# Performance work log

Hardware: AMD Instinct MI355X
Metric: run time of the kernel (lower is better)

Reference implementation:

```python
import jax, jax.numpy as jnp
import numpy as np

D_MODEL = 1024
NHEAD = 16
HEAD_DIM = D_MODEL // NHEAD
DFF = 4096
EPS = 1e-5


def _layernorm(x, g, b):
    mu = jnp.mean(x, axis=-1, keepdims=True)
    var = jnp.mean(jnp.square(x - mu), axis=-1, keepdims=True)
    return (x - mu) * jax.lax.rsqrt(var + EPS) * g + b


def setup_inputs() -> dict:
    key = jax.random.key(0)
    ks = jax.random.split(key, 20)
    B, S = 2, 2048
    s = 0.02
    inp = {
        "src": jax.random.normal(ks[0], (B, S, D_MODEL), jnp.float32),
        "recompute_idx": jnp.sort(jax.random.randint(ks[1], (409,), 0, S)),
        "cached_k": jax.random.normal(ks[2], (B, NHEAD, S, HEAD_DIM), jnp.float32),
        "cached_v": jax.random.normal(ks[3], (B, NHEAD, S, HEAD_DIM), jnp.float32),
        "Wq": jax.random.normal(ks[4], (D_MODEL, D_MODEL), jnp.float32) * s,
        "bq": jnp.zeros((D_MODEL,), jnp.float32),
        "Wk": jax.random.normal(ks[5], (D_MODEL, D_MODEL), jnp.float32) * s,
        "bk": jnp.zeros((D_MODEL,), jnp.float32),
        "Wv": jax.random.normal(ks[6], (D_MODEL, D_MODEL), jnp.float32) * s,
        "bv": jnp.zeros((D_MODEL,), jnp.float32),
        "Wo": jax.random.normal(ks[7], (D_MODEL, D_MODEL), jnp.float32) * s,
        "bo": jnp.zeros((D_MODEL,), jnp.float32),
        "W1": jax.random.normal(ks[8], (DFF, D_MODEL), jnp.float32) * s,
        "b1": jnp.zeros((DFF,), jnp.float32),
        "W2": jax.random.normal(ks[9], (D_MODEL, DFF), jnp.float32) * s,
        "b2": jnp.zeros((D_MODEL,), jnp.float32),
        "g1": jnp.ones((D_MODEL,), jnp.float32),
        "beta1": jnp.zeros((D_MODEL,), jnp.float32),
        "g2": jnp.ones((D_MODEL,), jnp.float32),
        "beta2": jnp.zeros((D_MODEL,), jnp.float32),
    }
    return inp


def reference(src, recompute_idx, cached_k, cached_v, Wq, bq, Wk, bk, Wv, bv,
              Wo, bo, W1, b1, W2, b2, g1, beta1, g2, beta2):
    B, S, D = src.shape
    H, hd = NHEAD, HEAD_DIM

    # Q for all tokens
    q = (src @ Wq.T + bq).reshape(B, S, H, hd).transpose(0, 2, 1, 3)  # [B,H,S,hd]

    # K/V recomputed only for selected tokens, scattered over cached KV
    src_rec = src[:, recompute_idx, :]  # [B,R,D]
    R = src_rec.shape[1]
    k_rec = (src_rec @ Wk.T + bk).reshape(B, R, H, hd).transpose(0, 2, 1, 3)
    v_rec = (src_rec @ Wv.T + bv).reshape(B, R, H, hd).transpose(0, 2, 1, 3)
    k_full = cached_k.at[:, :, recompute_idx, :].set(k_rec)  # [B,H,S,hd]
    v_full = cached_v.at[:, :, recompute_idx, :].set(v_rec)

    # attention over mixed cached/fresh KV
    scores = jnp.einsum('bhqd,bhkd->bhqk', q, k_full) / np.sqrt(hd).astype(src.dtype)
    probs = jax.nn.softmax(scores, axis=-1)
    attn = jnp.einsum('bhqk,bhkd->bhqd', probs, v_full)
    attn = attn.transpose(0, 2, 1, 3).reshape(B, S, D)
    attn = attn @ Wo.T + bo

    x = _layernorm(src + attn, g1, beta1)
    ff = jax.nn.relu(x @ W1.T + b1) @ W2.T + b2
    x = _layernorm(x + ff, g2, beta2)
    return x
```

## Files before the change

kernel.cpp:

```cpp
#include <hip/hip_runtime.h>
#include <hip/hip_bf16.h>

typedef __attribute__((ext_vector_type(4))) float f32x4;
typedef __attribute__((ext_vector_type(16))) float f32x16;
typedef __attribute__((ext_vector_type(8))) short s16x8;
typedef __attribute__((ext_vector_type(4))) short s16x4;
typedef __attribute__((ext_vector_type(2))) short s16x2;

typedef __attribute__((address_space(1))) const unsigned int guint;
typedef __attribute__((address_space(3))) unsigned int luint;

#define D_MODEL 1024
#define NHEAD 16
#define HEAD_DIM 64
#define DFF 4096
#define SEQ 2048
#define BATCH 2
#define QSCALE 0.18033688011112042f

__device__ __forceinline__ float b2f(short s) {
  union { unsigned int u; float f; } v;
  v.u = ((unsigned int)(unsigned short)s) << 16;
  return v.f;
}
__device__ __forceinline__ short f2b(float f) {
  __hip_bfloat16 h = __float2bfloat16(f);
  return *reinterpret_cast<short*>(&h);
}
__device__ __forceinline__ s16x8 cvt8(f32x4 a, f32x4 b) {
  s16x8 r;
  #pragma unroll
  for (int i = 0; i < 4; ++i) { r[i] = f2b(a[i]); r[i + 4] = f2b(b[i]); }
  return r;
}

template<int MODE>
__global__ __launch_bounds__(512, 2)
void gemm_ff8(const short* __restrict__ A, const short* __restrict__ W,
              const float* __restrict__ bias, short* __restrict__ out,
              int N, int K,
              short* __restrict__ pB, short* __restrict__ pC,
              short* __restrict__ pD)
{
  __shared__ short Al[2][16384];
  __shared__ short Bl[2][16384];

  const int tid  = threadIdx.x;
  const int lane = tid & 63, wave = tid >> 6;
  const int l31 = lane & 31, hi = lane >> 5;
  const int wm = (wave >> 2) * 128;
  const int wn = (wave & 3) * 64;

  const int nwg = gridDim.x * gridDim.y;
  int lid = blockIdx.y * gridDim.x + blockIdx.x;
  if ((nwg & 7) == 0) lid = (lid & 7) * (nwg >> 3) + (lid >> 3);
  const int bn = lid % gridDim.x, bm = lid / gridDim.x;

  const int Keff = (MODE == 1) ? (K >> 2) : K;
  const int kOff = (MODE == 1) ? (int)blockIdx.z * Keff : 0;

  const int srow = tid >> 3;
  const int scol = (((tid & 7) ^ ((tid >> 3) & 7)) * 8);
  const short* gA = A + ((long)(bm * 256) + srow) * K + kOff + scol;
  const short* gW = W + ((long)(bn * 256) + srow) * K + kOff + scol;
  const long slotG = 64L * K;

  auto stage = [&](int buf, int slot, int k0) {
    luint* dA = (luint*)((short*)Al + buf * 16384 + slot * 4096 + wave * 512);
    luint* dB = (luint*)((short*)Bl + buf * 16384 + slot * 4096 + wave * 512);
    __builtin_amdgcn_global_load_lds((guint*)(gA + slot * slotG + k0), dA, 16, 0, 0);
    __builtin_amdgcn_global_load_lds((guint*)(gW + slot * slotG + k0), dB, 16, 0, 0);
  };

  const int sw = l31 & 7;

  f32x16 acc[4][2] = {};

  #pragma unroll
  for (int s = 0; s < 4; ++s) stage(0, s, 0);

  const int nt = Keff / 64;
  int cur = 0;
  for (int t = 0; t < nt; ++t) {
    const int k1 = (t + 1) * 64;
    if (t + 1 < nt) {
      stage(cur ^ 1, 0, k1);
      asm volatile("s_waitcnt vmcnt(2)" ::: "memory");
    } else {
      asm volatile("s_waitcnt vmcnt(0)" ::: "memory");
    }
    __builtin_amdgcn_s_barrier();
    __builtin_amdgcn_sched_barrier(0);

    const short* Abuf = (const short*)Al + cur * 16384;
    const short* Bbuf = (const short*)Bl + cur * 16384;

    #pragma unroll
    for (int half = 0; half < 2; ++half) {
      s16x8 av[4][2], bv2[2][2];
      #pragma unroll
      for (int mf = 0; mf < 4; ++mf) {
        const int row = wm + mf * 32 + l31;
        #pragma unroll
        for (int k2 = 0; k2 < 2; ++k2) {
          const int kk = half * 2 + k2;
          av[mf][k2] = *(const s16x8*)(Abuf + row * 64 + (((kk * 2 + hi) ^ sw) << 3));
        }
      }
      #pragma unroll
      for (int nf = 0; nf < 2; ++nf) {
        const int row = wn + nf * 32 + l31;
        #pragma unroll
        for (int k2 = 0; k2 < 2; ++k2) {
          const int kk = half * 2 + k2;
          bv2[nf][k2] = *(const s16x8*)(Bbuf + row * 64 + (((kk * 2 + hi) ^ sw) << 3));
        }
      }
      if (t + 1 < nt) {
        stage(cur ^ 1, half * 2 + 1, k1);
        if (half == 1) stage(cur ^ 1, 2, k1);
      }

      __builtin_amdgcn_s_setprio(1);
      #pragma unroll
      for (int k2 = 0; k2 < 2; ++k2)
        #pragma unroll
        for (int mf = 0; mf < 4; ++mf)
          #pragma unroll
          for (int nf = 0; nf < 2; ++nf)
            acc[mf][nf] = __builtin_amdgcn_mfma_f32_32x32x16_bf16(
                av[mf][k2], bv2[nf][k2], acc[mf][nf], 0, 0, 0);
      __builtin_amdgcn_s_setprio(0);
    }

    __builtin_amdgcn_sched_barrier(0);
    __builtin_amdgcn_s_barrier();
    cur ^= 1;
  }

  short* oz = out;
  if (MODE == 1) {
    const int z = blockIdx.z;
    oz = (z == 0) ? out : (z == 1) ? pB : (z == 2) ? pC : pD;
  }
  #pragma unroll
  for (int mf = 0; mf < 4; ++mf) {
    #pragma unroll
    for (int nf = 0; nf < 2; ++nf) {
      const int gn = bn * 256 + wn + nf * 32 + l31;
      const float bvv = (MODE == 0) ? bias[gn] : 0.f;
      #pragma unroll
      for (int reg = 0; reg < 16; ++reg) {
        const int gm = bm * 256 + wm + mf * 32 + (reg & 3) + 8 * (reg >> 2) + 4 * hi;
        float v = acc[mf][nf][reg] + bvv;
        if (MODE == 0) v = v > 0.f ? v : 0.f;
        oz[(long)gm * N + gn] = f2b(v);
      }
    }
  }
}

template<int MODE, int BN, bool AF32, bool WF32>
__global__ __launch_bounds__(256, 3)
void gemm_nt(const void* __restrict__ Av, const void* __restrict__ Wv,
             const float* __restrict__ bias, short* __restrict__ out,
             int M, int N, int K,
             const int* __restrict__ idx, int R,
             const float* __restrict__ bias2, const float* __restrict__ bias3,
             short* __restrict__ pB, short* __restrict__ pC,
             short* __restrict__ pD)
{
  constexpr bool GLDS = (!AF32 && !WF32);
  constexpr int NI = BN / 32;

  const float* Af = (const float*)Av;
  const short* Ab = (const short*)Av;
  const float* Wf = (const float*)Wv;
  const short* Wb = (const short*)Wv;

  const int tid  = threadIdx.x;
  const int lane = tid & 63, wave = tid >> 6;
  const int g = lane >> 4, l15 = lane & 15;
  const int wm = (wave & 1) * 64, wn = (wave >> 1) * (BN / 2);

  const int nwg = gridDim.x * gridDim.y;
  int lid = blockIdx.y * gridDim.x + blockIdx.x;
  if ((nwg & 7) == 0) lid = (lid & 7) * (nwg >> 3) + (lid >> 3);
  const int bn = lid % gridDim.x;
  const int bm0 = lid / gridDim.x;

  int task = 0, bm = bm0, Mt = M;
  if (MODE == 8) {
    if (bm0 < 32)      { task = 0; bm = bm0;      Mt = M; }
    else if (bm0 < 39) { task = 1; bm = bm0 - 32; Mt = BATCH * R; }
    else               { task = 2; bm = bm0 - 39; Mt = BATCH * R; }
  }

  f32x4 acc[4][NI] = {};

  if constexpr (GLDS) {
    __shared__ short As[2][128][32];
    __shared__ short Bs[2][BN][32];

    const short* Wbase = Wb + ((MODE == 8) ? ((size_t)task << 20) : 0);
    const int nz   = (MODE == 6) ? gridDim.z : 1;
    const int Keff = K / nz;
    const int kOff = (MODE == 6) ? (int)blockIdx.z * Keff : 0;

    const int rA0 = wave * 16 + (lane >> 2);
    const int rA1 = rA0 + 64;
    const int cs = (((lane & 3) ^ ((lane >> 3) & 3)) * 8);

    auto arow = [&](int r) -> long {
      const int gm = bm * 128 + r;
      const int am = gm < Mt ? gm : Mt - 1;
      if (MODE == 8 && task > 0) {
        const int b0 = am / R;
        return (long)(b0 * SEQ + idx[am - b0 * R]);
      }
      return am;
    };
    const long aR0 = arow(rA0), aR1 = arow(rA1);
    const long wR0 = (long)bn * BN + rA0;

    const short* gA0 = Ab + aR0 * K + kOff + cs;
    const short* gA1 = Ab + aR1 * K + kOff + cs;
    const short* gB0 = Wbase + wR0 * K + kOff + cs;
    const short* gB1 = nullptr;
    if constexpr (BN == 128) gB1 = Wbase + ((long)bn * BN + rA1) * K + kOff + cs;

    auto stage = [&](int buf, int k0) {
      luint* lA0 = (luint*)((short*)As + buf * 4096 + wave * 512);
      luint* lA1 = (luint*)((short*)As + buf * 4096 + (4 + wave) * 512);
      luint* lB0 = (luint*)((short*)Bs + buf * (BN * 32) + wave * 512);
      __builtin_amdgcn_global_load_lds((guint*)(gA0 + k0), lA0, 16, 0, 0);
      __builtin_amdgcn_global_load_lds((guint*)(gA1 + k0), lA1, 16, 0, 0);
      __builtin_amdgcn_global_load_lds((guint*)(gB0 + k0), lB0, 16, 0, 0);
      if constexpr (BN == 128) {
        luint* lB1 = (luint*)((short*)Bs + buf * (BN * 32) + (4 + wave) * 512);
        __builtin_amdgcn_global_load_lds((guint*)(gB1 + k0), lB1, 16, 0, 0);
      }
    };

    const int rcol = ((g ^ ((l15 >> 1) & 3)) * 8);

    const int nt = Keff / 32;
    stage(0, 0);
    int cur = 0;
    for (int t = 0; t < nt; ++t) {
      if (t + 1 < nt) {
        stage(cur ^ 1, (t + 1) * 32);
        if constexpr (BN == 128) asm volatile("s_waitcnt vmcnt(4)" ::: "memory");
        else                     asm volatile("s_waitcnt vmcnt(3)" ::: "memory");
      } else {
        asm volatile("s_waitcnt vmcnt(0)" ::: "memory");
      }
      __builtin_amdgcn_s_barrier();
      __builtin_amdgcn_sched_barrier(0);

      s16x8 af[4], bf4[NI];
      #pragma unroll
      for (int mi = 0; mi < 4; ++mi)
        af[mi] = *(const s16x8*)&As[cur][wm + mi * 16 + l15][rcol];
      #pragma unroll
      for (int ni = 0; ni < NI; ++ni)
        bf4[ni] = *(const s16x8*)&Bs[cur][wn + ni * 16 + l15][rcol];
      #pragma unroll
      for (int mi = 0; mi < 4; ++mi)
        #pragma unroll
        for (int ni = 0; ni < NI; ++ni)
          acc[mi][ni] = __builtin_amdgcn_mfma_f32_16x16x32_bf16(af[mi], bf4[ni], acc[mi][ni], 0, 0, 0);

      __builtin_amdgcn_sched_barrier(0);
      __builtin_amdgcn_s_barrier();
      cur ^= 1;
    }
  } else {
    __shared__ short As[128][40];
    __shared__ short Bs[128][40];
    const int r0 = tid >> 1, c0 = (tid & 1) * 16;
    const int gm0 = bm * 128 + r0;
    const int am0 = gm0 < M ? gm0 : M - 1;
    long aRow0;
    if (MODE == 3 || MODE == 4) {
      const int b0 = am0 / R;
      aRow0 = (long)(b0 * SEQ + idx[am0 - b0 * R]);
    } else {
      aRow0 = am0;
    }
    const long wRow0 = bn * 128 + r0;

    for (int k0 = 0; k0 < K; k0 += 32) {
      __syncthreads();
      if (AF32) {
        f32x4 a0 = *(const f32x4*)(Af + aRow0 * K + k0 + c0);
        f32x4 a1 = *(const f32x4*)(Af + aRow0 * K + k0 + c0 + 4);
        f32x4 a2 = *(const f32x4*)(Af + aRow0 * K + k0 + c0 + 8);
        f32x4 a3 = *(const f32x4*)(Af + aRow0 * K + k0 + c0 + 12);
        *(s16x8*)&As[r0][c0]     = cvt8(a0, a1);
        *(s16x8*)&As[r0][c0 + 8] = cvt8(a2, a3);
      } else {
        *(s16x8*)&As[r0][c0]     = *(const s16x8*)(Ab + aRow0 * K + k0 + c0);
        *(s16x8*)&As[r0][c0 + 8] = *(const s16x8*)(Ab + aRow0 * K + k0 + c0 + 8);
      }
      if (WF32) {
        f32x4 w0 = *(const f32x4*)(Wf + wRow0 * K + k0 + c0);
        f32x4 w1 = *(const f32x4*)(Wf + wRow0 * K + k0 + c0 + 4);
        f32x4 w2 = *(const f32x4*)(Wf + wRow0 * K + k0 + c0 + 8);
        f32x4 w3 = *(const f32x4*)(Wf + wRow0 * K + k0 + c0 + 12);
        *(s16x8*)&Bs[r0][c0]     = cvt8(w0, w1);
        *(s16x8*)&Bs[r0][c0 + 8] = cvt8(w2, w3);
      } else {
        *(s16x8*)&Bs[r0][c0]     = *(const s16x8*)(Wb + wRow0 * K + k0 + c0);
        *(s16x8*)&Bs[r0][c0 + 8] = *(const s16x8*)(Wb + wRow0 * K + k0 + c0 + 8);
      }
      __syncthreads();

      s16x8 af[4], bf4[4];
      #pragma unroll
      for (int mi = 0; mi < 4; ++mi)
        af[mi] = *(const s16x8*)&As[wm + mi * 16 + l15][g * 8];
      #pragma unroll
      for (int ni = 0; ni < 4; ++ni)
        bf4[ni] = *(const s16x8*)&Bs[wn + ni * 16 + l15][g * 8];
      #pragma unroll
      for (int mi = 0; mi < 4; ++mi)
        #pragma unroll
        for (int ni = 0; ni < 4; ++ni)
          acc[mi][ni % NI] = __builtin_amdgcn_mfma_f32_16x16x32_bf16(af[mi], bf4[ni], acc[mi][ni % NI], 0, 0, 0);
    }
  }

  short* outz = out;
  if (MODE == 6) {
    const int z = blockIdx.z;
    outz = (z == 0) ? out : (z == 1) ? pB : (z == 2) ? pC : pD;
  }

  #pragma unroll
  for (int mi = 0; mi < 4; ++mi) {
    #pragma unroll
    for (int ni = 0; ni < NI; ++ni) {
      const int gn = bn * BN + wn + ni * 16 + l15;
      float bv;
      if (MODE == 6)      bv = 0.f;
      else if (MODE == 8) bv = (task == 0) ? bias[gn] : (task == 1) ? bias2[gn] : bias3[gn];
      else                bv = bias[gn];
      #pragma unroll
      for (int r = 0; r < 4; ++r) {
        const int gm = bm * 128 + wm + mi * 16 + g * 4 + r;
        if (MODE == 8) { if (gm >= Mt) continue; }
        else           { if (gm >= M)  continue; }
        float v = acc[mi][ni][r] + bv;
        if (MODE == 1) v = v > 0.f ? v : 0.f;
        if (MODE == 2) v *= QSCALE;
        if (MODE == 0 || MODE == 1) {
          out[(long)gm * N + gn] = f2b(v);
        } else if (MODE == 2) {
          const int b = gm >> 11, s = gm & (SEQ - 1);
          const int h = gn >> 6, d = gn & 63;
          out[(((long)(b * NHEAD + h)) * SEQ + s) * 64 + d] = f2b(v);
        } else if (MODE == 3) {
          const int b = gm / R, s = idx[gm - b * R];
          const int h = gn >> 6, d = gn & 63;
          out[(((long)(b * NHEAD + h)) * SEQ + s) * 64 + d] = f2b(v);
        } else if (MODE == 4) {
          const int b = gm / R, s = idx[gm - b * R];
          const int h = gn >> 6, d = gn & 63;
          out[(((long)(b * NHEAD + h)) * 64 + d) * SEQ + s] = f2b(v);
        } else if (MODE == 6) {
          outz[(long)gm * N + gn] = f2b(v);
        } else {
          const int h = gn >> 6, d = gn & 63;
          if (task == 0) {
            const int b = gm >> 11, s = gm & (SEQ - 1);
            out[(((long)(b * NHEAD + h)) * SEQ + s) * 64 + d] = f2b(v * QSCALE);
          } else if (task == 1) {
            const int b = gm / R, s = idx[gm - b * R];
            (out + (1L << 22))[(((long)(b * NHEAD + h)) * SEQ + s) * 64 + d] = f2b(v);
          } else {
            const int b = gm / R, s = idx[gm - b * R];
            (out + (1L << 23))[(((long)(b * NHEAD + h)) * 64 + d) * SEQ + s] = f2b(v);
          }
        }
      }
    }
  }
}

__global__ __launch_bounds__(256, 2)
void attn_fwd(const short* __restrict__ Q, const short* __restrict__ Kf,
              const short* __restrict__ Vt, short* __restrict__ out)
{
  __shared__ short Kl[2][64][64];
  __shared__ short Vl[2][64][64];

  const int tid  = threadIdx.x;
  const int lane = tid & 63, w = tid >> 6;
  const int g = lane >> 4, l15 = lane & 15;
  const int bh = blockIdx.x;
  const int qt = blockIdx.y;
  const int b  = bh >> 4, h = bh & 15;

  const long base = (long)bh * SEQ * 64;
  const int  q0   = qt * 128 + w * 32;

  s16x8 qf[2][2];
  #pragma unroll
  for (int mi = 0; mi < 2; ++mi)
    #pragma unroll
    for (int c = 0; c < 2; ++c)
      qf[mi][c] = *(const s16x8*)(Q + base + (long)(q0 + mi * 16 + l15) * 64 + c * 32 + g * 8);

  f32x4 o[2][4] = {};
  f32x4 os[2] = {};

  s16x8 ones;
  #pragma unroll
  for (int j = 0; j < 8; ++j) ones[j] = (short)0x3F80;

  auto ldsw = [](short (*buf)[64], int row, int slot) -> short* {
    return (short*)((char*)&buf[0][0] + row * 128 + ((slot ^ (row & 7)) << 4));
  };

  const int bo0 = w * 2048 + lane * 16;
  const int bo1 = bo0 + 1024;
  const int row0 = bo0 >> 7, ss0 = (((bo0 >> 4) & 7) ^ (row0 & 7));
  const int row1 = bo1 >> 7, ss1 = (((bo1 >> 4) & 7) ^ (row1 & 7));
  const short* gK0 = Kf + base + row0 * 64 + ss0 * 8;
  const short* gK1 = Kf + base + row1 * 64 + ss1 * 8;
  const short* gV0 = Vt + base + (long)row0 * SEQ + ss0 * 8;
  const short* gV1 = Vt + base + (long)row1 * SEQ + ss1 * 8;

  auto stage = [&](int buf, int t) {
    char* kb8 = (char*)&Kl[buf][0][0] + w * 2048;
    char* vb8 = (char*)&Vl[buf][0][0] + w * 2048;
    __builtin_amdgcn_global_load_lds((guint*)(gK0 + t * 4096), (luint*)kb8, 16, 0, 0);
    __builtin_amdgcn_global_load_lds((guint*)(gK1 + t * 4096), (luint*)(kb8 + 1024), 16, 0, 0);
    __builtin_amdgcn_global_load_lds((guint*)(gV0 + t * 64), (luint*)vb8, 16, 0, 0);
    __builtin_amdgcn_global_load_lds((guint*)(gV1 + t * 64), (luint*)(vb8 + 1024), 16, 0, 0);
  };

  stage(0, 0);
  int cur = 0;
  for (int t = 0; t < SEQ / 64; ++t) {
    if (t + 1 < SEQ / 64) {
      stage(cur ^ 1, t + 1);
      asm volatile("s_waitcnt vmcnt(4)" ::: "memory");
    } else {
      asm volatile("s_waitcnt vmcnt(0)" ::: "memory");
    }
    __builtin_amdgcn_s_barrier();
    __builtin_amdgcn_sched_barrier(0);

    f32x4 sc[2][4] = {};
    __builtin_amdgcn_s_setprio(1);
    #pragma unroll
    for (int c = 0; c < 2; ++c)
      #pragma unroll
      for (int n = 0; n < 4; ++n) {
        s16x8 kb = *(const s16x8*)ldsw(Kl[cur], n * 16 + l15, c * 4 + g);
        sc[0][n] = __builtin_amdgcn_mfma_f32_16x16x32_bf16(kb, qf[0][c], sc[0][n], 0, 0, 0);
        sc[1][n] = __builtin_amdgcn_mfma_f32_16x16x32_bf16(kb, qf[1][c], sc[1][n], 0, 0, 0);
      }
    __builtin_amdgcn_s_setprio(0);

    s16x8 pa[2][2];
    #pragma unroll
    for (int mi = 0; mi < 2; ++mi) {
      #pragma unroll
      for (int n = 0; n < 4; ++n)
        #pragma unroll
        for (int r = 0; r < 4; ++r) {
          float e;
          asm("v_exp_f32 %0, %1" : "=v"(e) : "v"(sc[mi][n][r]));
          sc[mi][n][r] = e;
        }
      unsigned int wpk[4][2];
      #pragma unroll
      for (int n = 0; n < 4; ++n)
        #pragma unroll
        for (int p = 0; p < 2; ++p)
          asm("v_cvt_pk_bf16_f32 %0, %1, %2"
              : "=v"(wpk[n][p]) : "v"(sc[mi][n][2 * p]), "v"(sc[mi][n][2 * p + 1]));
      #pragma unroll
      for (int c = 0; c < 2; ++c) {
        union { s16x8 v; unsigned int u[4]; } pu;
        #pragma unroll
        for (int p = 0; p < 2; ++p) {
          unsigned int a = wpk[2 * c][p], bb = wpk[2 * c + 1][p];
          asm volatile("v_permlane32_swap_b32 %0, %1" : "+v"(a), "+v"(bb));
          asm volatile("v_permlane16_swap_b32 %0, %1" : "+v"(a), "+v"(bb));
          pu.u[p]     = a;
          pu.u[2 + p] = bb;
        }
        pa[mi][c] = pu.v;
      }
    }

    __builtin_amdgcn_s_setprio(1);
    #pragma unroll
    for (int dt = 0; dt < 4; ++dt)
      #pragma unroll
      for (int c = 0; c < 2; ++c) {
        s16x8 vb = *(const s16x8*)ldsw(Vl[cur], dt * 16 + l15, c * 4 + g);
        o[0][dt] = __builtin_amdgcn_mfma_f32_16x16x32_bf16(pa[0][c], vb, o[0][dt], 0, 0, 0);
        o[1][dt] = __builtin_amdgcn_mfma_f32_16x16x32_bf16(pa[1][c], vb, o[1][dt], 0, 0, 0);
      }
    #pragma unroll
    for (int mi = 0; mi < 2; ++mi)
      #pragma unroll
      for (int c = 0; c < 2; ++c)
        os[mi] = __builtin_amdgcn_mfma_f32_16x16x32_bf16(pa[mi][c], ones, os[mi], 0, 0, 0);
    __builtin_amdgcn_s_setprio(0);

    __builtin_amdgcn_sched_barrier(0);
    __builtin_amdgcn_s_barrier();
    cur ^= 1;
  }

  float inv[2][4];
  #pragma unroll
  for (int mi = 0; mi < 2; ++mi)
    #pragma unroll
    for (int r = 0; r < 4; ++r)
      inv[mi][r] = 1.0f / os[mi][r];

  #pragma unroll
  for (int mi = 0; mi < 2; ++mi)
    #pragma unroll
    for (int dt = 0; dt < 4; ++dt)
      #pragma unroll
      for (int r = 0; r < 4; ++r) {
        const int q   = q0 + mi * 16 + g * 4 + r;
        const int col = h * 64 + dt * 16 + l15;
        out[((long)(b * SEQ + q)) * D_MODEL + col] = f2b(o[mi][dt][r] * inv[mi][r]);
      }
}

template<bool RES_F32, bool OUT_F32>
__global__ __launch_bounds__(256, 4)
void ln_ff2(const short* __restrict__ p0, const short* __restrict__ p1,
            const float* __restrict__ bias, const void* __restrict__ resv,
            const float* __restrict__ g, const float* __restrict__ beta,
            void* __restrict__ outv)
{
  __shared__ float red[8];
  const int row = blockIdx.x;
  const int tid = threadIdx.x;
  const int lane = tid & 63, w = tid >> 6;

  s16x4 v0 = *(const s16x4*)(p0 + (long)row * D_MODEL + tid * 4);
  s16x4 v1 = *(const s16x4*)(p1 + (long)row * D_MODEL + tid * 4);
  f32x4 vb = *(const f32x4*)(bias + tid * 4);
  float x[4];
  if (RES_F32) {
    f32x4 vr = *(const f32x4*)((const float*)resv + (long)row * D_MODEL + tid * 4);
    #pragma unroll
    for (int i = 0; i < 4; ++i) x[i] = vr[i] + b2f(v0[i]) + b2f(v1[i]) + vb[i];
  } else {
    s16x4 vr = *(const s16x4*)((const short*)resv + (long)row * D_MODEL + tid * 4);
    #pragma unroll
    for (int i = 0; i < 4; ++i) x[i] = b2f(vr[i]) + b2f(v0[i]) + b2f(v1[i]) + vb[i];
  }

  float sum = x[0] + x[1] + x[2] + x[3];
  #pragma unroll
  for (int msk = 32; msk >= 1; msk >>= 1) sum += __shfl_xor(sum, msk, 64);
  if (lane == 0) red[w] = sum;
  __syncthreads();
  sum = red[0] + red[1] + red[2] + red[3];
  const float mu = sum * (1.f / D_MODEL);

  float sq = 0.f;
  #pragma unroll
  for (int i = 0; i < 4; ++i) { float d = x[i] - mu; sq += d * d; }
  #pragma unroll
  for (int msk = 32; msk >= 1; msk >>= 1) sq += __shfl_xor(sq, msk, 64);
  if (lane == 0) red[4 + w] = sq;
  __syncthreads();
  sq = red[4] + red[5] + red[6] + red[7];
  const float rs = rsqrtf(sq * (1.f / D_MODEL) + 1e-5f);

  if (OUT_F32) {
    f32x4 ov;
    #pragma unroll
    for (int i = 0; i < 4; ++i) {
      const int c = tid * 4 + i;
      ov[i] = (x[i] - mu) * rs * g[c] + beta[c];
    }
    *(f32x4*)((float*)outv + (long)row * D_MODEL + tid * 4) = ov;
  } else {
    s16x4 ov;
    #pragma unroll
    for (int i = 0; i < 4; ++i) {
      const int c = tid * 4 + i;
      ov[i] = f2b((x[i] - mu) * rs * g[c] + beta[c]);
    }
    *(s16x4*)((short*)outv + (long)row * D_MODEL + tid * 4) = ov;
  }
}

__global__ __launch_bounds__(256, 4)
void ln_ff4(const short* __restrict__ p0, const short* __restrict__ p1,
            const short* __restrict__ p2, const short* __restrict__ p3,
            const float* __restrict__ bias, const short* __restrict__ xres,
            const float* __restrict__ g, const float* __restrict__ beta,
            float* __restrict__ outv)
{
  __shared__ float red[8];
  const int row = blockIdx.x;
  const int tid = threadIdx.x;
  const int lane = tid & 63, w = tid >> 6;

  s16x4 v0 = *(const s16x4*)(p0 + (long)row * D_MODEL + tid * 4);
  s16x4 v1 = *(const s16x4*)(p1 + (long)row * D_MODEL + tid * 4);
  s16x4 v2 = *(const s16x4*)(p2 + (long)row * D_MODEL + tid * 4);
  s16x4 v3 = *(const s16x4*)(p3 + (long)row * D_MODEL + tid * 4);
  s16x4 vx = *(const s16x4*)(xres + (long)row * D_MODEL + tid * 4);
  f32x4 vb = *(const f32x4*)(bias + tid * 4);
  float x[4];
  #pragma unroll
  for (int i = 0; i < 4; ++i)
    x[i] = b2f(vx[i]) + b2f(v0[i]) + b2f(v1[i]) + b2f(v2[i]) + b2f(v3[i]) + vb[i];

  float sum = x[0] + x[1] + x[2] + x[3];
  #pragma unroll
  for (int msk = 32; msk >= 1; msk >>= 1) sum += __shfl_xor(sum, msk, 64);
  if (lane == 0) red[w] = sum;
  __syncthreads();
  sum = red[0] + red[1] + red[2] + red[3];
  const float mu = sum * (1.f / D_MODEL);

  float sq = 0.f;
  #pragma unroll
  for (int i = 0; i < 4; ++i) { float d = x[i] - mu; sq += d * d; }
  #pragma unroll
  for (int msk = 32; msk >= 1; msk >>= 1) sq += __shfl_xor(sq, msk, 64);
  if (lane == 0) red[4 + w] = sq;
  __syncthreads();
  sq = red[4] + red[5] + red[6] + red[7];
  const float rs = rsqrtf(sq * (1.f / D_MODEL) + 1e-5f);

  f32x4 ov;
  #pragma unroll
  for (int i = 0; i < 4; ++i) {
    const int c = tid * 4 + i;
    ov[i] = (x[i] - mu) * rs * g[c] + beta[c];
  }
  *(f32x4*)(outv + (long)row * D_MODEL + tid * 4) = ov;
}

template<bool RES_F32, bool OUT_F32>
__global__ __launch_bounds__(256, 4)
void ln_res(const short* __restrict__ a, const void* __restrict__ resv,
            const float* __restrict__ g, const float* __restrict__ beta,
            void* __restrict__ outv)
{
  __shared__ float red[8];
  const int row = blockIdx.x;
  const int tid = threadIdx.x;
  const int lane = tid & 63, w = tid >> 6;

  s16x4 va = *(const s16x4*)(a + (long)row * D_MODEL + tid * 4);
  float x[4];
  if (RES_F32) {
    f32x4 vr = *(const f32x4*)((const float*)resv + (long)row * D_MODEL + tid * 4);
    #pragma unroll
    for (int i = 0; i < 4; ++i) x[i] = b2f(va[i]) + vr[i];
  } else {
    s16x4 vr = *(const s16x4*)((const short*)resv + (long)row * D_MODEL + tid * 4);
    #pragma unroll
    for (int i = 0; i < 4; ++i) x[i] = b2f(va[i]) + b2f(vr[i]);
  }
  float sum = x[0] + x[1] + x[2] + x[3];
  #pragma unroll
  for (int msk = 32; msk >= 1; msk >>= 1) sum += __shfl_xor(sum, msk, 64);
  if (lane == 0) red[w] = sum;
  __syncthreads();
  sum = red[0] + red[1] + red[2] + red[3];
  const float mu = sum * (1.f / D_MODEL);

  float sq = 0.f;
  #pragma unroll
  for (int i = 0; i < 4; ++i) { float d = x[i] - mu; sq += d * d; }
  #pragma unroll
  for (int msk = 32; msk >= 1; msk >>= 1) sq += __shfl_xor(sq, msk, 64);
  if (lane == 0) red[4 + w] = sq;
  __syncthreads();
  sq = red[4] + red[5] + red[6] + red[7];
  const float rs = rsqrtf(sq * (1.f / D_MODEL) + 1e-5f);

  if (OUT_F32) {
    f32x4 ov;
    #pragma unroll
    for (int i = 0; i < 4; ++i) {
      const int c = tid * 4 + i;
      ov[i] = (x[i] - mu) * rs * g[c] + beta[c];
    }
    *(f32x4*)((float*)outv + (long)row * D_MODEL + tid * 4) = ov;
  } else {
    s16x4 ov;
    #pragma unroll
    for (int i = 0; i < 4; ++i) {
      const int c = tid * 4 + i;
      ov[i] = f2b((x[i] - mu) * rs * g[c] + beta[c]);
    }
    *(s16x4*)((short*)outv + (long)row * D_MODEL + tid * 4) = ov;
  }
}

__global__ void cvt_all(const float* __restrict__ ck, const float* __restrict__ cv,
                        const float* __restrict__ src,
                        const float* __restrict__ Wq, const float* __restrict__ Wk,
                        const float* __restrict__ Wv, const float* __restrict__ Wo,
                        const float* __restrict__ W1, const float* __restrict__ W2,
                        short* __restrict__ k_ws, short* __restrict__ v_ws,
                        short* __restrict__ srcb,
                        short* __restrict__ Wqb, short* __restrict__ W1b,
                        short* __restrict__ W2b)
{
  for (int i = blockIdx.x * blockDim.x + threadIdx.x; i < 5767168;
       i += gridDim.x * blockDim.x) {
    if (i >= 5242880) {
      const int j = i - 5242880;
      const int bh = j >> 14;
      const int rem = j & 16383;
      const int d = rem & 63;
      const int s0 = (rem >> 6) << 3;
      s16x8 r;
      #pragma unroll
      for (int k = 0; k < 8; ++k)
        r[k] = f2b(cv[((long)bh * SEQ + s0 + k) * 64 + d]);
      *(s16x8*)(v_ws + ((long)bh * 64 + d) * SEQ + s0) = r;
      continue;
    }
    const float* s; short* d; int li;
    if      (i < 1048576) { s = ck;  d = k_ws;           li = i; }
    else if (i < 2097152) { s = src; d = srcb;           li = i - 1048576; }
    else if (i < 2359296) { s = Wq;  d = Wqb;            li = i - 2097152; }
    else if (i < 2621440) { s = Wk;  d = Wqb + 1048576;  li = i - 2359296; }
    else if (i < 2883584) { s = Wv;  d = Wqb + 2097152;  li = i - 2621440; }
    else if (i < 3145728) { s = Wo;  d = Wqb + 3145728;  li = i - 2883584; }
    else if (i < 4194304) { s = W1;  d = W1b;            li = i - 3145728; }
    else                  { s = W2;  d = W2b;            li = i - 4194304; }
    f32x4 v = *(const f32x4*)(s + (long)li * 4);
    s16x4 r;
    #pragma unroll
    for (int j = 0; j < 4; ++j) r[j] = f2b(v[j]);
    *(s16x4*)(d + (long)li * 4) = r;
  }
}

__global__ void cvt_v_t(const float* __restrict__ in, short* __restrict__ out)
{
  const int c2 = blockIdx.x * blockDim.x + threadIdx.x;
  const int bh = c2 >> 14;
  const int rem = c2 & 16383;
  const int d = rem & 63;
  const int s0 = (rem >> 6) << 3;
  s16x8 r;
  #pragma unroll
  for (int j = 0; j < 8; ++j)
    r[j] = f2b(in[((long)bh * SEQ + s0 + j) * 64 + d]);
  *(s16x8*)(out + ((long)bh * 64 + d) * SEQ + s0) = r;
}

__global__ void cvt_f32_bf16(const f32x4* __restrict__ in, s16x4* __restrict__ out, int n4)
{
  for (int i = blockIdx.x * blockDim.x + threadIdx.x; i < n4; i += gridDim.x * blockDim.x) {
    f32x4 v = in[i];
    s16x4 r;
    #pragma unroll
    for (int j = 0; j < 4; ++j) r[j] = f2b(v[j]);
    out[i] = r;
  }
}

extern "C" void kernel_launch(void* const* d_in, const int* in_sizes, int n_in,
                              void* d_out, int out_size, void* d_ws, size_t ws_size,
                              hipStream_t stream)
{
  const float* src = (const float*)d_in[0];
  const int*   idx = (const int*)  d_in[1];
  const float* ck  = (const float*)d_in[2];
  const float* cv  = (const float*)d_in[3];
  const float* Wq  = (const float*)d_in[4];
  const float* bq  = (const float*)d_in[5];
  const float* Wk  = (const float*)d_in[6];
  const float* bk  = (const float*)d_in[7];
  const float* Wv  = (const float*)d_in[8];
  const float* bv  = (const float*)d_in[9];
  const float* Wo  = (const float*)d_in[10];
  const float* bo  = (const float*)d_in[11];
  const float* W1  = (const float*)d_in[12];
  const float* b1  = (const float*)d_in[13];
  const float* W2  = (const float*)d_in[14];
  const float* b2  = (const float*)d_in[15];
  const float* g1  = (const float*)d_in[16];
  const float* be1 = (const float*)d_in[17];
  const float* g2  = (const float*)d_in[18];
  const float* be2 = (const float*)d_in[19];
  float* out = (float*)d_out;

  char* ws = (char*)d_ws;
  const size_t SZ = (size_t)4096 * 1024 * 2;
  short* x_ws    = (short*)(ws);
  short* proj_ws = (short*)(ws + SZ);
  short* q_ws    = (short*)(ws + 2 * SZ);
  short* k_ws    = (short*)(ws + 3 * SZ);
  short* v_ws    = (short*)(ws + 4 * SZ);
  short* attn_ws = (short*)(ws + 5 * SZ);
  short* h_ws    = (short*)(ws + 2 * SZ);
  short* W1b     = (short*)(ws + 6 * SZ);
  short* W2b     = (short*)(ws + 7 * SZ);
  short* srcb    = (short*)(ws + 8 * SZ);
  short* Wqb     = (short*)(ws + 9 * SZ);
  const bool big = ws_size >= 10 * SZ;

  const int M = BATCH * SEQ;
  const int R = 409;
  const int Mr = BATCH * R;
  const int nkv4 = BATCH * NHEAD * SEQ * HEAD_DIM / 4;

  if (big) {
    cvt_all<<<2048, 256, 0, stream>>>(ck, cv, src, Wq, Wk, Wv, Wo, W1, W2,
                                      k_ws, v_ws, srcb, Wqb, W1b, W2b);
    gemm_nt<8, 64, false, false><<<dim3(16, 46), 256, 0, stream>>>(
        srcb, Wqb, bq, q_ws, M, 1024, 1024, idx, R, bk, bv, nullptr, nullptr, nullptr);
    attn_fwd<<<dim3(BATCH * NHEAD, SEQ / 128), 256, 0, stream>>>(q_ws, k_ws, v_ws, attn_ws);
    gemm_nt<6, 64, false, false><<<dim3(16, 32, 2), 256, 0, stream>>>(
        attn_ws, Wqb + 3145728, nullptr, proj_ws, M, 1024, 1024, nullptr, 0,
        nullptr, nullptr, q_ws, nullptr, nullptr);
    ln_ff2<true, false><<<4096, 256, 0, stream>>>(proj_ws, q_ws, bo, src, g1, be1, x_ws);
    gemm_ff8<0><<<dim3(16, 16), 512, 0, stream>>>(
        x_ws, W1b, b1, h_ws, DFF, 1024, nullptr, nullptr, nullptr);
    gemm_ff8<1><<<dim3(4, 16, 4), 512, 0, stream>>>(
        h_ws, W2b, nullptr, proj_ws, 1024, 4096, W1b, srcb, Wqb);
    ln_ff4<<<4096, 256, 0, stream>>>(proj_ws, W1b, srcb, Wqb, b2, x_ws, g2, be2, out);
  } else {
    cvt_f32_bf16<<<2048, 256, 0, stream>>>((const f32x4*)ck, (s16x4*)k_ws, nkv4);
    cvt_v_t<<<2048, 256, 0, stream>>>(cv, v_ws);
    gemm_nt<2, 128, true, true><<<dim3(8, 32), 256, 0, stream>>>(
        src, Wq, bq, q_ws, M, 1024, 1024, nullptr, 0, nullptr, nullptr, nullptr, nullptr, nullptr);
    gemm_nt<3, 128, true, true><<<dim3(8, 7), 256, 0, stream>>>(
        src, Wk, bk, k_ws, Mr, 1024, 1024, idx, R, nullptr, nullptr, nullptr, nullptr, nullptr);
    gemm_nt<4, 128, true, true><<<dim3(8, 7), 256, 0, stream>>>(
        src, Wv, bv, v_ws, Mr, 1024, 1024, idx, R, nullptr, nullptr, nullptr, nullptr, nullptr);
    attn_fwd<<<dim3(BATCH * NHEAD, SEQ / 128), 256, 0, stream>>>(q_ws, k_ws, v_ws, attn_ws);
    gemm_nt<0, 128, false, true><<<dim3(8, 32), 256, 0, stream>>>(
        attn_ws, Wo, bo, proj_ws, M, 1024, 1024, nullptr, 0, nullptr, nullptr, nullptr, nullptr, nullptr);
    ln_res<true, false><<<4096, 256, 0, stream>>>(proj_ws, src, g1, be1, x_ws);
    gemm_nt<1, 128, false, true><<<dim3(32, 32), 256, 0, stream>>>(
        x_ws, W1, b1, h_ws, M, DFF, 1024, nullptr, 0, nullptr, nullptr, nullptr, nullptr, nullptr);
    gemm_nt<0, 128, false, true><<<dim3(8, 32), 256, 0, stream>>>(
        h_ws, W2, b2, proj_ws, M, 1024, DFF, nullptr, 0, nullptr, nullptr, nullptr, nullptr, nullptr);
    ln_res<false, true><<<4096, 256, 0, stream>>>(proj_ws, x_ws, g2, be2, out);
  }
}
```

Measured before the change: 224.3 us.

## Double GEMM K-tile depth to 64 with new LDS swizzle and MFMA priority

The GLDS GEMM path now stages 64-wide K slices per iteration instead of 32, using a new XOR swizzle over 8 chunks and per-wave row assignment for global-to-LDS loads. This halves the number of barrier-synchronised iterations and doubles the MFMA work between barriers, amortising sync and wait overhead. It also raises wave priority around the MFMA block with s_setprio. In exchange LDS use doubles, which may lower occupancy, and more loads are in flight per stage.

```diff
diff --git a/kernel.cpp b/kernel.cpp
--- a/kernel.cpp
+++ b/kernel.cpp
@@ -199,17 +199,16 @@
   f32x4 acc[4][NI] = {};
 
   if constexpr (GLDS) {
-    __shared__ short As[2][128][32];
-    __shared__ short Bs[2][BN][32];
+    __shared__ short As[2][128][64];
+    __shared__ short Bs[2][BN][64];
 
     const short* Wbase = Wb + ((MODE == 8) ? ((size_t)task << 20) : 0);
     const int nz   = (MODE == 6) ? gridDim.z : 1;
     const int Keff = K / nz;
     const int kOff = (MODE == 6) ? (int)blockIdx.z * Keff : 0;
 
-    const int rA0 = wave * 16 + (lane >> 2);
-    const int rA1 = rA0 + 64;
-    const int cs = (((lane & 3) ^ ((lane >> 3) & 3)) * 8);
+    const int srow8 = lane >> 3;
+    const int scol  = ((lane & 7) ^ srow8) * 8;
 
     auto arow = [&](int r) -> long {
       const int gm = bm * 128 + r;
@@ -220,56 +219,68 @@
       }
       return am;
     };
-    const long aR0 = arow(rA0), aR1 = arow(rA1);
-    const long wR0 = (long)bn * BN + rA0;
-
-    const short* gA0 = Ab + aR0 * K + kOff + cs;
-    const short* gA1 = Ab + aR1 * K + kOff + cs;
-    const short* gB0 = Wbase + wR0 * K + kOff + cs;
-    const short* gB1 = nullptr;
-    if constexpr (BN == 128) gB1 = Wbase + ((long)bn * BN + rA1) * K + kOff + cs;
+
+    const short* gAp[4];
+    #pragma unroll
+    for (int j = 0; j < 4; ++j)
+      gAp[j] = Ab + arow(wave * 32 + j * 8 + srow8) * K + kOff + scol;
+    constexpr int BI = BN / 32;
+    const short* gBp[BI];
+    #pragma unroll
+    for (int j = 0; j < BI; ++j)
+      gBp[j] = Wbase + ((long)bn * BN + wave * (BN / 4) + j * 8 + srow8) * K + kOff + scol;
 
     auto stage = [&](int buf, int k0) {
-      luint* lA0 = (luint*)((short*)As + buf * 4096 + wave * 512);
-      luint* lA1 = (luint*)((short*)As + buf * 4096 + (4 + wave) * 512);
-      luint* lB0 = (luint*)((short*)Bs + buf * (BN * 32) + wave * 512);
-      __builtin_amdgcn_global_load_lds((guint*)(gA0 + k0), lA0, 16, 0, 0);
-      __builtin_amdgcn_global_load_lds((guint*)(gA1 + k0), lA1, 16, 0, 0);
-      __builtin_amdgcn_global_load_lds((guint*)(gB0 + k0), lB0, 16, 0, 0);
-      if constexpr (BN == 128) {
-        luint* lB1 = (luint*)((short*)Bs + buf * (BN * 32) + (4 + wave) * 512);
-        __builtin_amdgcn_global_load_lds((guint*)(gB1 + k0), lB1, 16, 0, 0);
+      #pragma unroll
+      for (int j = 0; j < 4; ++j) {
+        luint* d = (luint*)((short*)As + buf * 8192 + wave * 2048 + j * 512);
+        __builtin_amdgcn_global_load_lds((guint*)(gAp[j] + k0), d, 16, 0, 0);
+      }
+      #pragma unroll
+      for (int j = 0; j < BI; ++j) {
+        luint* d = (luint*)((short*)Bs + buf * (BN * 64) + wave * (BN * 16) + j * 512);
+        __builtin_amdgcn_global_load_lds((guint*)(gBp[j] + k0), d, 16, 0, 0);
       }
     };
 
-    const int rcol = ((g ^ ((l15 >> 1) & 3)) * 8);
-
-    const int nt = Keff / 32;
+    const int sw = l15 & 7;
+
+    const int nt = Keff / 64;
     stage(0, 0);
     int cur = 0;
     for (int t = 0; t < nt; ++t) {
       if (t + 1 < nt) {
-        stage(cur ^ 1, (t + 1) * 32);
-        if constexpr (BN == 128) asm volatile("s_waitcnt vmcnt(4)" ::: "memory");
-        else                     asm volatile("s_waitcnt vmcnt(3)" ::: "memory");
+        stage(cur ^ 1, (t + 1) * 64);
+        if constexpr (BN == 128) asm volatile("s_waitcnt vmcnt(8)" ::: "memory");
+        else                     asm volatile("s_waitcnt vmcnt(6)" ::: "memory");
       } else {
         asm volatile("s_waitcnt vmcnt(0)" ::: "memory");
       }
       __builtin_amdgcn_s_barrier();
       __builtin_amdgcn_sched_barrier(0);
 
-      s16x8 af[4], bf4[NI];
+      s16x8 af[4][2], bf[NI][2];
       #pragma unroll
       for (int mi = 0; mi < 4; ++mi)
-        af[mi] = *(const s16x8*)&As[cur][wm + mi * 16 + l15][rcol];
+        #pragma unroll
+        for (int kk = 0; kk < 2; ++kk)
+          af[mi][kk] = *(const s16x8*)&As[cur][wm + mi * 16 + l15][(((kk * 4 + g) ^ sw) << 3)];
       #pragma unroll
       for (int ni = 0; ni < NI; ++ni)
-        bf4[ni] = *(const s16x8*)&Bs[cur][wn + ni * 16 + l15][rcol];
-      #pragma unroll
-      for (int mi = 0; mi < 4; ++mi)
-        #pragma unroll
-        for (int ni = 0; ni < NI; ++ni)
-          acc[mi][ni] = __builtin_amdgcn_mfma_f32_16x16x32_bf16(af[mi], bf4[ni], acc[mi][ni], 0, 0, 0);
+        #pragma unroll
+        for (int kk = 0; kk < 2; ++kk)
+          bf[ni][kk] = *(const s16x8*)&Bs[cur][wn + ni * 16 + l15][(((kk * 4 + g) ^ sw) << 3)];
+
+      __builtin_amdgcn_s_setprio(1);
+      #pragma unroll
+      for (int kk = 0; kk < 2; ++kk)
+        #pragma unroll
+        for (int mi = 0; mi < 4; ++mi)
+          #pragma unroll
+          for (int ni = 0; ni < NI; ++ni)
+            acc[mi][ni] = __builtin_amdgcn_mfma_f32_16x16x32_bf16(
+                af[mi][kk], bf[ni][kk], acc[mi][ni], 0, 0, 0);
+      __builtin_amdgcn_s_setprio(0);
 
       __builtin_amdgcn_sched_barrier(0);
       __builtin_amdgcn_s_barrier();
```

New measurement: 220.8 us (median of 2 runs). No clear change (-1.5%).
